# Optimization experiments

Measured on AMD Instinct MI355X. Metric: run time of the kernel, lower is better.

## Reference

```python
import jax, jax.numpy as jnp
import numpy as np

WS = 8  # window size (hardcoded in original forward)

def _window_partition(x, ws=WS):
    b, c, h, w = x.shape
    ph = (-h) % ws
    pw = (-w) % ws
    x = jnp.pad(x, ((0, 0), (0, 0), (0, ph), (0, pw)), mode='reflect')
    H, W = h + ph, w + pw
    # matches torch .view(b,c,ws,H//ws,ws,W//ws).permute(0,1,2,4,3,5)
    x = x.reshape(b, c, ws, H // ws, ws, W // ws)
    x = x.transpose(0, 1, 2, 4, 3, 5).reshape(b, c * ws * ws, H // ws, W // ws)
    return x, h, w, c, H // ws

def _l2norm_dim1(x):
    # F.normalize(x, p=2) defaults to dim=1 (token axis for [b, L, d]), eps=1e-12
    n = jnp.sqrt(jnp.sum(x * x, axis=1, keepdims=True))
    return x / jnp.maximum(n, 1e-12)

def _forward(q, k, v):
    b = q.shape[0]
    qp, qh, qw, qc, patch = _window_partition(q)
    kp, _, _, _, _ = _window_partition(k)
    vp, _, _, _, _ = _window_partition(v)
    d = qp.shape[1]  # c * ws * ws
    qt = qp.transpose(0, 2, 3, 1).reshape(b, -1, d)  # [b, L, d]
    kt = kp.transpose(0, 2, 3, 1).reshape(b, -1, d)
    vt = vp.transpose(0, 2, 3, 1).reshape(b, -1, d)
    _q = _l2norm_dim1(qt)
    _k = _l2norm_dim1(kt)
    _v = _l2norm_dim1(vt)
    sim = jnp.einsum('bld,bmd->blm', _q, _k) * (d ** -0.5)  # [b, L, L]
    out = jnp.einsum('blm,bmd->bld', jax.nn.softmax(sim, axis=-1), _v)
    # window_reverse
    L = out.shape[1]
    ws = WS
    x = out.reshape(b, patch, L // patch, qc, ws, ws)
    x = x.transpose(0, 3, 4, 1, 5, 2)  # (b, c, ws, patch, ws, L//patch)
    H = ws * patch
    x = x.reshape(b, qc, H, -1)
    return x[:, :, :qh, :qw]

def setup_inputs() -> dict:
    key = jax.random.key(0)
    kq, kk, kv = jax.random.split(key, 3)
    shape = (8, 32, 252, 252)
    return {
        'q': jax.random.normal(kq, shape, dtype=jnp.float32),
        'k': jax.random.normal(kk, shape, dtype=jnp.float32),
        'v': jax.random.normal(kv, shape, dtype=jnp.float32),
    }

def reference(q, k, v):
    return _forward(q, k, v)
```

## Files before the change

kernel.cpp:

```cpp
#include <hip/hip_runtime.h>
#include <cstdint>
#include <cstddef>


typedef __bf16 bf16x8 __attribute__((ext_vector_type(8)));
typedef float  f32x4  __attribute__((ext_vector_type(4)));

__device__ __forceinline__ unsigned int f2bf(float f) {
  unsigned int u = __builtin_bit_cast(unsigned int, f);
  u += 0x7FFFu + ((u >> 16) & 1u);
  return u >> 16;
}
__device__ __forceinline__ float bf2f(unsigned short h) {
  return __builtin_bit_cast(float, (unsigned int)h << 16);
}

__device__ __forceinline__ void load_lds16(const void* g, void* l) {
  __builtin_amdgcn_global_load_lds(
      (const __attribute__((address_space(1))) void*)g,
      (__attribute__((address_space(3))) void*)l, 16, 0, 0);
}

__global__ void norm_kernel(const float* __restrict__ q,
                            const float* __restrict__ k,
                            const float* __restrict__ v,
                            float* __restrict__ scales) {
  int bx = blockIdx.x;
  int t = bx >> 10;
  int b = (bx >> 7) & 7;
  int c = (bx >> 2) & 31;
  int g = bx & 3;
  const float* x = (t == 0) ? q : (t == 1) ? k : v;
  const float* base = x + ((size_t)b * 32 + c) * 63504;

  int tid = threadIdx.x;
  int w = tid;
  bool active = (w < 252);
  float cw = ((unsigned)(w - 247) <= 3u) ? 2.f : 1.f;

  float acc0 = 0.f, acc1 = 0.f;
  if (active) {
    int h0 = g * 64;
    int nrows = (g == 3) ? 60 : 64;
    #pragma unroll 8
    for (int hh = 0; hh < 64; hh++) {
      if (hh < nrows) {
        int h = h0 + hh;
        float val = base[(size_t)h * 252 + w];
        float v2 = val * val;
        if ((unsigned)(h - 247) <= 3u) v2 *= 2.f;
        if (hh < 32) acc0 += v2; else acc1 += v2;
      }
    }
  }
  acc0 *= cw; acc1 *= cw;

  __shared__ float red[512];
  red[tid] = acc0;
  red[256 + tid] = acc1;
  __syncthreads();
  if (tid < 16) {
    int i0loc = tid >> 3;
    int j0    = tid & 7;
    float s = 0.f;
    #pragma unroll
    for (int e = 0; e < 32; e++) s += red[i0loc * 256 + j0 * 32 + e];
    float sc = 1.0f / fmaxf(sqrtf(s), 1e-12f);
    int i0 = g * 2 + i0loc;
    scales[((size_t)(t * 8 + b)) * 2048 + i0 * 256 + j0 * 32 + c] = sc;
  }
}

__global__ void pack_qk_kernel(const float* __restrict__ q,
                               const float* __restrict__ k,
                               const float* __restrict__ scales,
                               unsigned short* __restrict__ Qh,
                               unsigned short* __restrict__ Kh) {
  int bx = blockIdx.x;
  int t   = bx >> 11;
  int rem = bx & 2047;
  int b   = rem >> 8;
  int i0  = (rem >> 5) & 7;
  int i1  = rem & 31;
  const float* x = (t == 0) ? q : k;

  __shared__ float tf[32 * 257];
  __shared__ float sclt[256];

  int tid = threadIdx.x;
  sclt[(tid & 31) * 8 + (tid >> 5)] =
      scales[((size_t)(t * 8 + b)) * 2048 + i0 * 256 + tid];

  int h  = i0 * 32 + i1;
  int hs = (h < 252) ? h : 502 - h;
  const float* xb = x + (size_t)b * 32 * 63504 + (size_t)hs * 252;

  #pragma unroll
  for (int r = 0; r < 8; r++) {
    int c     = r * 4 + (tid >> 6);
    int chunk = tid & 63;
    const float* src = xb + (size_t)c * 63504;
    int j0 = chunk >> 3, cq = chunk & 7;
    float4 vv;
    if (chunk < 63) {
      vv = *(const float4*)&src[chunk * 4];
    } else {
      vv.x = src[250]; vv.y = src[249]; vv.z = src[248]; vv.w = src[247];
    }
    float* row = &tf[c * 257 + j0 * 32];
    int p = cq * 4 + j0;
    row[p & 31]       = vv.x;
    row[(p + 1) & 31] = vv.y;
    row[(p + 2) & 31] = vv.z;
    row[(p + 3) & 31] = vv.w;
  }
  __syncthreads();

  int p0  = (tid * 8) & 255;
  int j0w = p0 >> 5;
  int c0  = p0 & 31;
  float scl_r[8];
  #pragma unroll
  for (int m = 0; m < 8; m++) scl_r[m] = sclt[(c0 + m) * 8 + j0w];

  unsigned short* X = ((t == 0) ? Qh : Kh) + (size_t)b * 1024 * 2048;
  #pragma unroll
  for (int r = 0; r < 4; r++) {
    int j1 = r * 8 + (tid >> 5);
    int rot = (j1 + j0w) & 31;
    unsigned int ov[4];
    #pragma unroll
    for (int m = 0; m < 4; m++) {
      float lo = tf[(c0 + 2 * m)     * 257 + j0w * 32 + rot] * scl_r[2 * m];
      float hi = tf[(c0 + 2 * m + 1) * 257 + j0w * 32 + rot] * scl_r[2 * m + 1];
      ov[m] = f2bf(lo) | (f2bf(hi) << 16);
    }
    int l = i1 * 32 + j1;
    uint4 o4; o4.x = ov[0]; o4.y = ov[1]; o4.z = ov[2]; o4.w = ov[3];
    *(uint4*)&X[(size_t)l * 2048 + i0 * 256 + p0] = o4;
  }
}

__global__ void pack_v_kernel(const float* __restrict__ v,
                              unsigned short* __restrict__ Vt) {
  int bx = blockIdx.x;
  int b  = bx >> 8;
  int i0 = (bx >> 5) & 7;
  int i1 = bx & 31;
  int h  = i0 * 32 + i1;
  int hs = (h < 252) ? h : 502 - h;
  const float* src = v + (size_t)b * 32 * 63504 + (size_t)hs * 252;
  unsigned short* dst = Vt + (size_t)b * 2048 * 1024
                           + (size_t)(i0 * 256) * 1024 + i1 * 32;

  int tid = threadIdx.x;
  int j1c = tid & 3;
  int c   = (tid >> 2) & 31;
  int j0g = tid >> 7;
  const float* s = src + (size_t)c * 63504;

  #pragma unroll
  for (int jj = 0; jj < 4; jj++) {
    int j0 = j0g * 4 + jj;
    int w0 = j0 * 32 + j1c * 8;
    float f0, f1, f2, f3, f4, f5, f6, f7;
    if (w0 + 8 <= 252) {
      float4 a = *(const float4*)&s[w0];
      float4 bq = *(const float4*)&s[w0 + 4];
      f0 = a.x; f1 = a.y; f2 = a.z; f3 = a.w;
      f4 = bq.x; f5 = bq.y; f6 = bq.z; f7 = bq.w;
    } else {
      float4 a = *(const float4*)&s[244];
      float4 bq = *(const float4*)&s[248];
      f0 = bq.x; f1 = bq.y; f2 = bq.z; f3 = bq.w;
      f4 = bq.z; f5 = bq.y; f6 = bq.x; f7 = a.w;
    }
    uint4 o;
    o.x = f2bf(f0) | (f2bf(f1) << 16);
    o.y = f2bf(f2) | (f2bf(f3) << 16);
    o.z = f2bf(f4) | (f2bf(f5) << 16);
    o.w = f2bf(f6) | (f2bf(f7) << 16);
    *(uint4*)&dst[(size_t)(j0 * 32 + c) * 1024 + j1c * 8] = o;
  }
}

template <int MODE>
__global__ __launch_bounds__(256, 4)
void gemm_nt(const unsigned short* __restrict__ A,
             const unsigned short* __restrict__ B,
             int K, int Asb, int Bsb, void* __restrict__ Cout, float scale,
             const float* __restrict__ sv) {
  __shared__ unsigned short lA[128 * 64];
  __shared__ unsigned short lB[128 * 64];
  __shared__ float svb[(MODE == 1) ? 128 : 1];

  const int tid  = threadIdx.x;
  const int lane = tid & 63;
  const int wave = tid >> 6;
  const int ln15 = lane & 15;
  const int q4   = lane >> 4;
  const int wm   = wave >> 1;
  const int wn   = wave & 1;
  const int m0   = blockIdx.y * 128;
  const int n0   = blockIdx.x * 128;
  const unsigned short* Ab = A + (size_t)blockIdx.z * Asb;
  const unsigned short* Bb = B + (size_t)blockIdx.z * Bsb;

  if (MODE == 1 && tid < 128)
    svb[tid] = sv[(size_t)blockIdx.z * 2048 + m0 + tid];

  const int srow = lane >> 3;
  const int kcp  = lane & 7;
  const int kcl  = kcp ^ srow;

  f32x4 acc[4][4] = {};

  for (int k0 = 0; k0 < K; k0 += 64) {
    #pragma unroll
    for (int r = 0; r < 4; r++) {
      int rowg = wave * 32 + r * 8;
      int row  = rowg + srow;
      load_lds16(&Ab[(size_t)(m0 + row) * K + k0 + kcl * 8], &lA[rowg * 64]);
      load_lds16(&Bb[(size_t)(n0 + row) * K + k0 + kcl * 8], &lB[rowg * 64]);
    }
    __syncthreads();
    #pragma unroll
    for (int kk = 0; kk < 2; kk++) {
      bf16x8 af[4], bfr[4];
      #pragma unroll
      for (int mt = 0; mt < 4; mt++) {
        int row = wm * 64 + mt * 16 + ln15;
        int pc  = (kk * 4 + q4) ^ (row & 7);
        af[mt] = *(const bf16x8*)&lA[row * 64 + pc * 8];
      }
      #pragma unroll
      for (int nt = 0; nt < 4; nt++) {
        int row = wn * 64 + nt * 16 + ln15;
        int pc  = (kk * 4 + q4) ^ (row & 7);
        bfr[nt] = *(const bf16x8*)&lB[row * 64 + pc * 8];
      }
      #pragma unroll
      for (int mt = 0; mt < 4; mt++)
        #pragma unroll
        for (int nt = 0; nt < 4; nt++)
          acc[mt][nt] = __builtin_amdgcn_mfma_f32_16x16x32_bf16(
              af[mt], bfr[nt], acc[mt][nt], 0, 0, 0);
    }
    __syncthreads();
  }

  if (MODE == 0) {
    unsigned short* Sb = (unsigned short*)Cout + (size_t)blockIdx.z * 1024 * 1024;
    #pragma unroll
    for (int mt = 0; mt < 4; mt++) {
      #pragma unroll
      for (int nt = 0; nt < 4; nt++) {
        int col = n0 + wn * 64 + nt * 16 + ln15;
        #pragma unroll
        for (int rg = 0; rg < 4; rg++) {
          int rowi = m0 + wm * 64 + mt * 16 + q4 * 4 + rg;
          Sb[(size_t)rowi * 1024 + col] = (unsigned short)f2bf(acc[mt][nt][rg] * scale);
        }
      }
    }
  } else {
    float* Ob = (float*)Cout;
    int bb = blockIdx.z;
    #pragma unroll
    for (int mt = 0; mt < 4; mt++) {
      #pragma unroll
      for (int nt = 0; nt < 4; nt++) {
        int l  = n0 + wn * 64 + nt * 16 + ln15;
        int i1 = l >> 5, j1 = l & 31;
        #pragma unroll
        for (int rg = 0; rg < 4; rg++) {
          int rloc = wm * 64 + mt * 16 + q4 * 4 + rg;
          int dp = m0 + rloc;
          int c  = dp & 31;
          int j0 = (dp >> 5) & 7;
          int i0 = dp >> 8;
          int h = i0 * 32 + i1;
          int w = j0 * 32 + j1;
          if (h < 252 && w < 252)
            Ob[(((size_t)bb * 32 + c) * 252 + h) * 252 + w] =
                acc[mt][nt][rg] * svb[rloc];
        }
      }
    }
  }
}

__global__ void softmax_kernel(unsigned short* __restrict__ S) {
  unsigned short* row = S + (size_t)blockIdx.x * 1024;
  int tid  = threadIdx.x;
  int lane = tid & 63;
  int wid  = tid >> 6;

  uint2 u = *(const uint2*)&row[tid * 4];
  float x0 = bf2f((unsigned short)(u.x & 0xFFFF));
  float x1 = bf2f((unsigned short)(u.x >> 16));
  float x2 = bf2f((unsigned short)(u.y & 0xFFFF));
  float x3 = bf2f((unsigned short)(u.y >> 16));

  __shared__ float red[8];
  float mx = fmaxf(fmaxf(x0, x1), fmaxf(x2, x3));
  #pragma unroll
  for (int off = 32; off > 0; off >>= 1) mx = fmaxf(mx, __shfl_down(mx, off));
  if (lane == 0) red[wid] = mx;
  __syncthreads();
  if (tid == 0)
    red[4] = fmaxf(fmaxf(red[0], red[1]), fmaxf(red[2], red[3]));
  __syncthreads();
  float bm = red[4];

  float e0 = __expf(x0 - bm), e1 = __expf(x1 - bm);
  float e2 = __expf(x2 - bm), e3 = __expf(x3 - bm);
  float s = e0 + e1 + e2 + e3;
  #pragma unroll
  for (int off = 32; off > 0; off >>= 1) s += __shfl_down(s, off);
  if (lane == 0) red[wid] = s;
  __syncthreads();
  if (tid == 0) red[5] = 1.0f / (red[0] + red[1] + red[2] + red[3]);
  __syncthreads();
  float inv = red[5];

  unsigned int o0 = f2bf(e0 * inv) | (f2bf(e1 * inv) << 16);
  unsigned int o1 = f2bf(e2 * inv) | (f2bf(e3 * inv) << 16);
  uint2 o; o.x = o0; o.y = o1;
  *(uint2*)&row[tid * 4] = o;
}

extern "C" void kernel_launch(void* const* d_in, const int* in_sizes, int n_in,
                              void* d_out, int out_size, void* d_ws, size_t ws_size,
                              hipStream_t stream) {
  const float* q = (const float*)d_in[0];
  const float* k = (const float*)d_in[1];
  const float* v = (const float*)d_in[2];
  float* out = (float*)d_out;

  char* ws = (char*)d_ws;
  float* scales = (float*)ws;
  unsigned short* Qh = (unsigned short*)(ws + 196608);
  unsigned short* Kh = Qh + (size_t)8 * 1024 * 2048;
  unsigned short* Vt = Kh + (size_t)8 * 1024 * 2048;
  unsigned short* S  = Vt + (size_t)8 * 2048 * 1024;

  const float SIM_SCALE = 0.02209708691207961f;
  const float* sv = scales + (size_t)2 * 8 * 2048;

  norm_kernel<<<3072, 256, 0, stream>>>(q, k, v, scales);
  pack_qk_kernel<<<4096, 256, 0, stream>>>(q, k, scales, Qh, Kh);
  pack_v_kernel<<<2048, 256, 0, stream>>>(v, Vt);
  gemm_nt<0><<<dim3(8, 8, 8), 256, 0, stream>>>(
      Qh, Kh, 2048, 1024 * 2048, 1024 * 2048, (void*)S, SIM_SCALE, nullptr);
  softmax_kernel<<<8192, 256, 0, stream>>>(S);
  gemm_nt<1><<<dim3(8, 16, 8), 256, 0, stream>>>(
      Vt, S, 1024, 2048 * 1024, 1024 * 1024, (void*)out, 1.0f, sv);
}
```

Measured before the change: 426.2 us.

## Fuse norm computation into QK packing and compute V norms from packed bf16

Norm and pack passes for Q/K are merged into one kernel. It packs unscaled bf16 rows, accumulates per-column sum of squares while loading, then rescales its own output slice in place. V norms are now computed by a separate small kernel reading the packed bf16 Vt, so V no longer needs a separate fp32 norm pass. GEMM launches switch to a flattened 1D grid with batch in the low bits, which changes block scheduling order. The trade-offs are an extra read-modify-write of the Q/K buffers, a pack grid cut from 4096 to 512 blocks (with a serial 32-row loop and two barriers per row), and V norms taken from bf16-rounded values.

Result: faster. 376.7 us (-11.6%).

```diff
diff --git a/kernel.cpp b/kernel.cpp
--- a/kernel.cpp
+++ b/kernel.cpp
@@ -11,8 +11,8 @@
   u += 0x7FFFu + ((u >> 16) & 1u);
   return u >> 16;
 }
-__device__ __forceinline__ float bf2f(unsigned short h) {
-  return __builtin_bit_cast(float, (unsigned int)h << 16);
+__device__ __forceinline__ float bf2f(unsigned int h) {
+  return __builtin_bit_cast(float, h << 16);
 }
 
 __device__ __forceinline__ void load_lds16(const void* g, void* l) {
@@ -21,123 +21,110 @@
       (__attribute__((address_space(3))) void*)l, 16, 0, 0);
 }
 
-__global__ void norm_kernel(const float* __restrict__ q,
-                            const float* __restrict__ k,
-                            const float* __restrict__ v,
-                            float* __restrict__ scales) {
-  int bx = blockIdx.x;
-  int t = bx >> 10;
-  int b = (bx >> 7) & 7;
-  int c = (bx >> 2) & 31;
-  int g = bx & 3;
-  const float* x = (t == 0) ? q : (t == 1) ? k : v;
-  const float* base = x + ((size_t)b * 32 + c) * 63504;
+__global__ __launch_bounds__(256)
+void pack_qk_fused(const float* __restrict__ q, const float* __restrict__ k,
+                   unsigned short* __restrict__ Qh,
+                   unsigned short* __restrict__ Kh) {
+  int bx  = blockIdx.x;
+  int t   = bx >> 8;
+  int b   = (bx >> 5) & 7;
+  int i0  = (bx >> 2) & 7;
+  int j0g = bx & 3;
+  const float* xb = (t ? k : q) + (size_t)b * 32 * 63504;
+
+  __shared__ float tf[32 * 65];
+  __shared__ float red[512];
+  __shared__ float sclt[64];
 
   int tid = threadIdx.x;
-  int w = tid;
-  bool active = (w < 252);
-  float cw = ((unsigned)(w - 247) <= 3u) ? 2.f : 1.f;
-
-  float acc0 = 0.f, acc1 = 0.f;
-  if (active) {
-    int h0 = g * 64;
-    int nrows = (g == 3) ? 60 : 64;
-    #pragma unroll 8
-    for (int hh = 0; hh < 64; hh++) {
-      if (hh < nrows) {
-        int h = h0 + hh;
-        float val = base[(size_t)h * 252 + w];
-        float v2 = val * val;
-        if ((unsigned)(h - 247) <= 3u) v2 *= 2.f;
-        if (hh < 32) acc0 += v2; else acc1 += v2;
-      }
-    }
-  }
-  acc0 *= cw; acc1 *= cw;
-
-  __shared__ float red[512];
-  red[tid] = acc0;
-  red[256 + tid] = acc1;
-  __syncthreads();
-  if (tid < 16) {
-    int i0loc = tid >> 3;
-    int j0    = tid & 7;
+  int ch  = tid & 15;
+  int c2  = tid >> 4;
+
+  int wbase = j0g * 64 + ch * 4;
+  float we[4];
+  #pragma unroll
+  for (int e = 0; e < 4; e++) {
+    int w = wbase + e;
+    we[e] = (w >= 252) ? 0.f : (((unsigned)(w - 247) <= 3u) ? 2.f : 1.f);
+  }
+  bool tail = (wbase == 252);
+
+  float pa = 0.f, pb = 0.f;
+  unsigned short* X = (t ? Kh : Qh) + (size_t)b * 1024 * 2048;
+
+  int gsub = tid & 7;
+  int gj1  = tid >> 3;
+  int gjl  = gsub >> 2;
+  int gc0  = (gsub & 3) * 8;
+
+  for (int i1 = 0; i1 < 32; i1++) {
+    int h  = i0 * 32 + i1;
+    int hs = (h < 252) ? h : 502 - h;
+    float rw = (h >= 252) ? 0.f : (((unsigned)(h - 247) <= 3u) ? 2.f : 1.f);
+    const float* rowp = xb + (size_t)hs * 252;
+
+    #pragma unroll
+    for (int it = 0; it < 2; it++) {
+      int c = c2 + it * 16;
+      const float* src = rowp + (size_t)c * 63504;
+      float4 vv;
+      if (!tail) {
+        vv = *(const float4*)&src[wbase];
+      } else {
+        vv.x = src[250]; vv.y = src[249]; vv.z = src[248]; vv.w = src[247];
+      }
+      float s = rw * (we[0] * vv.x * vv.x + we[1] * vv.y * vv.y +
+                      we[2] * vv.z * vv.z + we[3] * vv.w * vv.w);
+      if (it == 0) pa += s; else pb += s;
+      float* dst = &tf[c * 65 + ch * 4];
+      dst[0] = vv.x; dst[1] = vv.y; dst[2] = vv.z; dst[3] = vv.w;
+    }
+    __syncthreads();
+    {
+      int pos = gjl * 32 + gj1;
+      unsigned int ov[4];
+      #pragma unroll
+      for (int m = 0; m < 4; m++) {
+        unsigned int lo = f2bf(tf[(gc0 + 2 * m)     * 65 + pos]);
+        unsigned int hi = f2bf(tf[(gc0 + 2 * m + 1) * 65 + pos]);
+        ov[m] = lo | (hi << 16);
+      }
+      int l = i1 * 32 + gj1;
+      uint4 o4; o4.x = ov[0]; o4.y = ov[1]; o4.z = ov[2]; o4.w = ov[3];
+      *(uint4*)&X[(size_t)l * 2048 + i0 * 256 + j0g * 64 + gsub * 8] = o4;
+    }
+    __syncthreads();
+  }
+
+  red[tid] = pa; red[256 + tid] = pb;
+  __syncthreads();
+  if (tid < 64) {
+    int c = tid & 31, jl = tid >> 5;
+    int base = (c & 15) * 16 + jl * 8 + ((c >= 16) ? 256 : 0);
     float s = 0.f;
     #pragma unroll
-    for (int e = 0; e < 32; e++) s += red[i0loc * 256 + j0 * 32 + e];
-    float sc = 1.0f / fmaxf(sqrtf(s), 1e-12f);
-    int i0 = g * 2 + i0loc;
-    scales[((size_t)(t * 8 + b)) * 2048 + i0 * 256 + j0 * 32 + c] = sc;
-  }
-}
-
-__global__ void pack_qk_kernel(const float* __restrict__ q,
-                               const float* __restrict__ k,
-                               const float* __restrict__ scales,
-                               unsigned short* __restrict__ Qh,
-                               unsigned short* __restrict__ Kh) {
-  int bx = blockIdx.x;
-  int t   = bx >> 11;
-  int rem = bx & 2047;
-  int b   = rem >> 8;
-  int i0  = (rem >> 5) & 7;
-  int i1  = rem & 31;
-  const float* x = (t == 0) ? q : k;
-
-  __shared__ float tf[32 * 257];
-  __shared__ float sclt[256];
-
-  int tid = threadIdx.x;
-  sclt[(tid & 31) * 8 + (tid >> 5)] =
-      scales[((size_t)(t * 8 + b)) * 2048 + i0 * 256 + tid];
-
-  int h  = i0 * 32 + i1;
-  int hs = (h < 252) ? h : 502 - h;
-  const float* xb = x + (size_t)b * 32 * 63504 + (size_t)hs * 252;
-
-  #pragma unroll
-  for (int r = 0; r < 8; r++) {
-    int c     = r * 4 + (tid >> 6);
-    int chunk = tid & 63;
-    const float* src = xb + (size_t)c * 63504;
-    int j0 = chunk >> 3, cq = chunk & 7;
-    float4 vv;
-    if (chunk < 63) {
-      vv = *(const float4*)&src[chunk * 4];
-    } else {
-      vv.x = src[250]; vv.y = src[249]; vv.z = src[248]; vv.w = src[247];
-    }
-    float* row = &tf[c * 257 + j0 * 32];
-    int p = cq * 4 + j0;
-    row[p & 31]       = vv.x;
-    row[(p + 1) & 31] = vv.y;
-    row[(p + 2) & 31] = vv.z;
-    row[(p + 3) & 31] = vv.w;
-  }
-  __syncthreads();
-
-  int p0  = (tid * 8) & 255;
-  int j0w = p0 >> 5;
-  int c0  = p0 & 31;
-  float scl_r[8];
-  #pragma unroll
-  for (int m = 0; m < 8; m++) scl_r[m] = sclt[(c0 + m) * 8 + j0w];
-
-  unsigned short* X = ((t == 0) ? Qh : Kh) + (size_t)b * 1024 * 2048;
-  #pragma unroll
-  for (int r = 0; r < 4; r++) {
-    int j1 = r * 8 + (tid >> 5);
-    int rot = (j1 + j0w) & 31;
-    unsigned int ov[4];
-    #pragma unroll
-    for (int m = 0; m < 4; m++) {
-      float lo = tf[(c0 + 2 * m)     * 257 + j0w * 32 + rot] * scl_r[2 * m];
-      float hi = tf[(c0 + 2 * m + 1) * 257 + j0w * 32 + rot] * scl_r[2 * m + 1];
-      ov[m] = f2bf(lo) | (f2bf(hi) << 16);
-    }
-    int l = i1 * 32 + j1;
-    uint4 o4; o4.x = ov[0]; o4.y = ov[1]; o4.z = ov[2]; o4.w = ov[3];
-    *(uint4*)&X[(size_t)l * 2048 + i0 * 256 + p0] = o4;
+    for (int u = 0; u < 8; u++) s += red[base + u];
+    sclt[c * 2 + jl] = 1.f / fmaxf(sqrtf(s), 1e-12f);
+  }
+  __syncthreads();
+
+  {
+    float sc[8];
+    #pragma unroll
+    for (int m = 0; m < 8; m++) sc[m] = sclt[(gc0 + m) * 2 + gjl];
+    unsigned short* basep = &X[i0 * 256 + j0g * 64 + gsub * 8];
+    int lb = tid >> 3;
+    #pragma unroll 4
+    for (int it = 0; it < 32; it++) {
+      size_t off = (size_t)(it * 32 + lb) * 2048;
+      uint4 u = *(uint4*)&basep[off];
+      uint4 o;
+      o.x = f2bf(bf2f(u.x & 0xFFFF) * sc[0]) | (f2bf(bf2f(u.x >> 16) * sc[1]) << 16);
+      o.y = f2bf(bf2f(u.y & 0xFFFF) * sc[2]) | (f2bf(bf2f(u.y >> 16) * sc[3]) << 16);
+      o.z = f2bf(bf2f(u.z & 0xFFFF) * sc[4]) | (f2bf(bf2f(u.z >> 16) * sc[5]) << 16);
+      o.w = f2bf(bf2f(u.w & 0xFFFF) * sc[6]) | (f2bf(bf2f(u.w >> 16) * sc[7]) << 16);
+      *(uint4*)&basep[off] = o;
+    }
   }
 }
 
@@ -184,6 +171,32 @@
   }
 }
 
+__global__ void sv_kernel(const unsigned short* __restrict__ Vt,
+                          float* __restrict__ sv) {
+  int bx = blockIdx.x;
+  int b  = bx >> 5;
+  int dg = bx & 31;
+  int tid = threadIdx.x;
+  int r  = tid >> 2;
+  int qd = tid & 3;
+  const unsigned short* row =
+      Vt + (size_t)b * 2048 * 1024 + (size_t)(dg * 64 + r) * 1024;
+  float s = 0.f;
+  #pragma unroll 8
+  for (int it = 0; it < 32; it++) {
+    uint4 u = *(const uint4*)&row[it * 32 + qd * 8];
+    float a0 = bf2f(u.x & 0xFFFF), a1 = bf2f(u.x >> 16);
+    float a2 = bf2f(u.y & 0xFFFF), a3 = bf2f(u.y >> 16);
+    float a4 = bf2f(u.z & 0xFFFF), a5 = bf2f(u.z >> 16);
+    float a6 = bf2f(u.w & 0xFFFF), a7 = bf2f(u.w >> 16);
+    s += a0*a0 + a1*a1 + a2*a2 + a3*a3 + a4*a4 + a5*a5 + a6*a6 + a7*a7;
+  }
+  s += __shfl_down(s, 2, 4);
+  s += __shfl_down(s, 1, 4);
+  if (qd == 0)
+    sv[(size_t)b * 2048 + dg * 64 + r] = 1.f / fmaxf(sqrtf(s), 1e-12f);
+}
+
 template <int MODE>
 __global__ __launch_bounds__(256, 4)
 void gemm_nt(const unsigned short* __restrict__ A,
@@ -194,6 +207,12 @@
   __shared__ unsigned short lB[128 * 64];
   __shared__ float svb[(MODE == 1) ? 128 : 1];
 
+  const int flat = blockIdx.x;
+  const int zz   = flat & 7;
+  const int rr   = flat >> 3;
+  const int my   = rr >> 3;
+  const int nx   = rr & 7;
+
   const int tid  = threadIdx.x;
   const int lane = tid & 63;
   const int wave = tid >> 6;
@@ -201,13 +220,13 @@
   const int q4   = lane >> 4;
   const int wm   = wave >> 1;
   const int wn   = wave & 1;
-  const int m0   = blockIdx.y * 128;
-  const int n0   = blockIdx.x * 128;
-  const unsigned short* Ab = A + (size_t)blockIdx.z * Asb;
-  const unsigned short* Bb = B + (size_t)blockIdx.z * Bsb;
+  const int m0   = my * 128;
+  const int n0   = nx * 128;
+  const unsigned short* Ab = A + (size_t)zz * Asb;
+  const unsigned short* Bb = B + (size_t)zz * Bsb;
 
   if (MODE == 1 && tid < 128)
-    svb[tid] = sv[(size_t)blockIdx.z * 2048 + m0 + tid];
+    svb[tid] = sv[(size_t)zz * 2048 + m0 + tid];
 
   const int srow = lane >> 3;
   const int kcp  = lane & 7;
@@ -250,7 +269,7 @@
   }
 
   if (MODE == 0) {
-    unsigned short* Sb = (unsigned short*)Cout + (size_t)blockIdx.z * 1024 * 1024;
+    unsigned short* Sb = (unsigned short*)Cout + (size_t)zz * 1024 * 1024;
     #pragma unroll
     for (int mt = 0; mt < 4; mt++) {
       #pragma unroll
@@ -265,7 +284,6 @@
     }
   } else {
     float* Ob = (float*)Cout;
-    int bb = blockIdx.z;
     #pragma unroll
     for (int mt = 0; mt < 4; mt++) {
       #pragma unroll
@@ -282,7 +300,7 @@
           int h = i0 * 32 + i1;
           int w = j0 * 32 + j1;
           if (h < 252 && w < 252)
-            Ob[(((size_t)bb * 32 + c) * 252 + h) * 252 + w] =
+            Ob[(((size_t)zz * 32 + c) * 252 + h) * 252 + w] =
                 acc[mt][nt][rg] * svb[rloc];
         }
       }
@@ -297,10 +315,10 @@
   int wid  = tid >> 6;
 
   uint2 u = *(const uint2*)&row[tid * 4];
-  float x0 = bf2f((unsigned short)(u.x & 0xFFFF));
-  float x1 = bf2f((unsigned short)(u.x >> 16));
-  float x2 = bf2f((unsigned short)(u.y & 0xFFFF));
-  float x3 = bf2f((unsigned short)(u.y >> 16));
+  float x0 = bf2f(u.x & 0xFFFF);
+  float x1 = bf2f(u.x >> 16);
+  float x2 = bf2f(u.y & 0xFFFF);
+  float x3 = bf2f(u.y >> 16);
 
   __shared__ float red[8];
   float mx = fmaxf(fmaxf(x0, x1), fmaxf(x2, x3));
@@ -339,21 +357,20 @@
   float* out = (float*)d_out;
 
   char* ws = (char*)d_ws;
-  float* scales = (float*)ws;
+  float* sv = (float*)ws;
   unsigned short* Qh = (unsigned short*)(ws + 196608);
   unsigned short* Kh = Qh + (size_t)8 * 1024 * 2048;
   unsigned short* Vt = Kh + (size_t)8 * 1024 * 2048;
   unsigned short* S  = Vt + (size_t)8 * 2048 * 1024;
 
   const float SIM_SCALE = 0.02209708691207961f;
-  const float* sv = scales + (size_t)2 * 8 * 2048;
-
-  norm_kernel<<<3072, 256, 0, stream>>>(q, k, v, scales);
-  pack_qk_kernel<<<4096, 256, 0, stream>>>(q, k, scales, Qh, Kh);
+
+  pack_qk_fused<<<512, 256, 0, stream>>>(q, k, Qh, Kh);
   pack_v_kernel<<<2048, 256, 0, stream>>>(v, Vt);
-  gemm_nt<0><<<dim3(8, 8, 8), 256, 0, stream>>>(
+  sv_kernel<<<256, 256, 0, stream>>>(Vt, sv);
+  gemm_nt<0><<<512, 256, 0, stream>>>(
       Qh, Kh, 2048, 1024 * 2048, 1024 * 2048, (void*)S, SIM_SCALE, nullptr);
   softmax_kernel<<<8192, 256, 0, stream>>>(S);
-  gemm_nt<1><<<dim3(8, 16, 8), 256, 0, stream>>>(
+  gemm_nt<1><<<1024, 256, 0, stream>>>(
       Vt, S, 1024, 2048 * 1024, 1024 * 1024, (void*)out, 1.0f, sv);
 }
```
